# Kernel tuning notes

Measured on AMD Instinct MI355X. Metric: run time of the kernel, lower is better.

The kernel has to match this reference:

```python
import jax, jax.numpy as jnp
import numpy as np

T = 0.07  # temperature from __init__ default


def setup_inputs() -> dict:
    key = jax.random.key(0)
    ks = jax.random.split(key, 5)
    B, D, H, E = 4096, 2048, 2048, 128
    init = lambda k, shp, fan: jax.random.normal(k, shp, dtype=jnp.float32) * (1.0 / np.sqrt(fan))
    return {
        "input1": jax.random.normal(ks[0], (B, D), dtype=jnp.float32),
        "input2": jax.random.normal(ks[1], (B, D), dtype=jnp.float32),
        "W0": init(ks[2], (D, H), D), "b0": jnp.zeros((H,), jnp.float32),
        "W1": init(ks[3], (H, H), H), "b1": jnp.zeros((H,), jnp.float32),
        "W2": init(ks[4], (H, E), H), "b2": jnp.zeros((E,), jnp.float32),
    }


def _mlp(x, W0, b0, W1, b1, W2, b2):
    # Linear -> ReLU -> Linear -> Linear (ReLU only between hidden layers)
    x = jax.nn.relu(x @ W0 + b0)
    x = x @ W1 + b1
    return x @ W2 + b2


def reference(input1, input2, W0, b0, W1, b1, W2, b2):
    B = input1.shape[0]
    e1 = _mlp(input1, W0, b0, W1, b1, W2, b2)
    e2 = _mlp(input2, W0, b0, W1, b1, W2, b2)
    feats = jnp.stack([e1, e2], axis=1)                       # [B, 2, E]
    feats = feats / jnp.linalg.norm(feats, axis=2, keepdims=True)
    # view(N,2,dim).permute(1,0,2).reshape(2N,dim): view0 rows then view1 rows
    f = jnp.concatenate([feats[:, 0], feats[:, 1]], axis=0)   # [2B, E]
    N2 = 2 * B
    sim = (f @ f.T) / T                                        # [2B, 2B]
    idx = jnp.arange(N2)
    pos = sim[idx, (idx + B) % N2]                             # partner view similarity
    # exclude self-similarity (diagonal) from the logsumexp denominator
    sim = jnp.where(jnp.eye(N2, dtype=bool), jnp.float32(-1e9), sim)
    # CE with positive at index 0 of [pos, negatives] == -pos + logsumexp(non-self)
    loss = jnp.mean(jax.nn.logsumexp(sim, axis=1) - pos)
    return loss
```

## Files before the change

kernel.cpp:

```cpp
#include <hip/hip_runtime.h>
#include <stdint.h>

typedef float f32x4 __attribute__((ext_vector_type(4)));
typedef float f32x16 __attribute__((ext_vector_type(16)));
typedef __bf16 bf16x8 __attribute__((ext_vector_type(8)));
typedef unsigned short u16;
typedef unsigned int u32;

#define INVT 14.285714285714286f
#define L2E  1.4426950408889634f

__device__ __forceinline__ u16 f2bf(float f) {
  u32 u = __float_as_uint(f);
  u32 r = (u + 0x7fffu + ((u >> 16) & 1u)) >> 16;
  return (u16)r;
}
__device__ __forceinline__ float bf2f(u16 h) { return __uint_as_float(((u32)h) << 16); }

__device__ __forceinline__ void g2l16(const void* g, void* l) {
  auto gp = reinterpret_cast<__attribute__((address_space(1))) uint32_t*>(
      reinterpret_cast<uintptr_t>(g));
  auto lp = reinterpret_cast<__attribute__((address_space(3))) uint32_t*>(
      reinterpret_cast<uintptr_t>(l));
  __builtin_amdgcn_global_load_lds(gp, lp, 16, 0, 0);
}

__global__ __launch_bounds__(256) void k_prep(const float* __restrict__ in1,
                                              const float* __restrict__ in2,
                                              u16* __restrict__ Xb,
                                              const float* __restrict__ w0, u16* __restrict__ w0t,
                                              const float* __restrict__ w1, u16* __restrict__ w1t,
                                              const float* __restrict__ w2, u16* __restrict__ w2t) {
  const int bid = blockIdx.x;
  if (bid < 16384) {
    int i = (bid * 256 + threadIdx.x) * 4;
    float4 v;
    if (i < 8388608) v = *(const float4*)(in1 + i);
    else             v = *(const float4*)(in2 + (i - 8388608));
    ushort4 p;
    p.x = f2bf(v.x); p.y = f2bf(v.y); p.z = f2bf(v.z); p.w = f2bf(v.w);
    *(ushort4*)(Xb + i) = p;
    return;
  }
  __shared__ float t[64][65];
  const float* in; u16* out; int R, C, r0, c0;
  if (bid < 18432) {
    const int f = bid - 16384;
    const int z = f >> 10, rem = f & 1023;
    in = z ? w1 : w0; out = z ? w1t : w0t; R = 2048; C = 2048;
    r0 = (rem >> 5) * 64; c0 = (rem & 31) * 64;
  } else {
    const int f = bid - 18432;
    in = w2; out = w2t; R = 2048; C = 128;
    r0 = (f >> 1) * 64; c0 = (f & 1) * 64;
  }
#pragma unroll
  for (int p = 0; p < 16; ++p) {
    int idx = p * 256 + threadIdx.x;
    int r = idx >> 6, c = idx & 63;
    t[r][c] = in[(size_t)(r0 + r) * C + (c0 + c)];
  }
  __syncthreads();
#pragma unroll
  for (int p = 0; p < 16; ++p) {
    int idx = p * 256 + threadIdx.x;
    int c = idx >> 6, r = idx & 63;
    out[(size_t)(c0 + c) * R + (r0 + r)] = f2bf(t[r][c]);
  }
}

__global__ __launch_bounds__(256, 2) void k_gemm(const u16* __restrict__ A, const u16* __restrict__ Bt,
                                                 const float* __restrict__ bias, u16* __restrict__ C,
                                                 int M, int N, int K, int relu) {
  __shared__ __align__(16) u16 sm[36864];
  const int tid = threadIdx.x;
  const int l = tid & 63, w = tid >> 6;
  const int wm = w >> 1, wn = w & 1;
  const int m0 = blockIdx.y * 256, n0 = blockIdx.x * 128;

  const int kb = ((l & 3) ^ ((l >> 3) & 3)) * 16;
  const char* gA = (const char*)(A + (size_t)(m0 + w * 64 + (l >> 2)) * K) + kb;
  const char* gB = (const char*)(Bt + (size_t)(n0 + w * 32 + (l >> 2)) * K) + kb;
  const size_t chRows = (size_t)16 * K * 2;

  auto issue = [&](int kcB, int stg) {
    char* base = (char*)sm + stg * 24576;
    char* dA = base + (w * 4) * 1024 + l * 16;
    char* dB = base + 16384 + (w * 2) * 1024 + l * 16;
#pragma unroll
    for (int j = 0; j < 4; ++j) g2l16(gA + j * chRows + kcB, dA + j * 1024);
#pragma unroll
    for (int j = 0; j < 2; ++j) g2l16(gB + j * chRows + kcB, dB + j * 1024);
  };

  const int lm = l & 31;
  const int c0 = l >> 5;
  const int sw = (lm >> 1) & 3;

  f32x16 acc[4][2] = {};

  auto compute = [&](int stg) {
    const u16* As = sm + stg * 12288;
    const u16* Bs = As + 8192;
#pragma unroll
    for (int t = 0; t < 2; ++t) {
      const int cc = (((t << 1) + c0) ^ sw) * 8;
      bf16x8 a4[4], b2[2];
#pragma unroll
      for (int fm = 0; fm < 4; ++fm)
        a4[fm] = *(const bf16x8*)(As + (wm * 128 + fm * 32 + lm) * 32 + cc);
#pragma unroll
      for (int fn = 0; fn < 2; ++fn)
        b2[fn] = *(const bf16x8*)(Bs + (wn * 64 + fn * 32 + lm) * 32 + cc);
#pragma unroll
      for (int fm = 0; fm < 4; ++fm)
#pragma unroll
        for (int fn = 0; fn < 2; ++fn)
          acc[fm][fn] = __builtin_amdgcn_mfma_f32_32x32x16_bf16(a4[fm], b2[fn],
                                                                acc[fm][fn], 0, 0, 0);
    }
  };

  const int NK = K >> 5;
  issue(0, 0);
  issue(64, 1);
  int st = 0;
  for (int kt = 0; kt < NK; ++kt) {
    if (kt + 1 < NK) asm volatile("s_waitcnt vmcnt(6)" ::: "memory");
    else             asm volatile("s_waitcnt vmcnt(0)" ::: "memory");
    asm volatile("s_barrier" ::: "memory");
    if (kt + 2 < NK) {
      int stp = st + 2; if (stp >= 3) stp -= 3;
      issue((kt + 2) * 64, stp);
    }
    compute(st);
    ++st; if (st == 3) st = 0;
  }

  const int colb = n0 + wn * 64 + lm;
  const int rowb = m0 + wm * 128 + 4 * c0;
#pragma unroll
  for (int fn = 0; fn < 2; ++fn) {
    const float b = bias[colb + fn * 32];
#pragma unroll
    for (int fm = 0; fm < 4; ++fm)
#pragma unroll
      for (int g = 0; g < 4; ++g)
#pragma unroll
        for (int rr = 0; rr < 4; ++rr) {
          float v = acc[fm][fn][g * 4 + rr] + b;
          if (relu) v = fmaxf(v, 0.0f);
          C[(size_t)(rowb + fm * 32 + g * 8 + rr) * N + colb + fn * 32] = f2bf(v);
        }
  }
}

__global__ __launch_bounds__(256, 2) void k_gemm_sk(const u16* __restrict__ A, const u16* __restrict__ Bt,
                                                    float* __restrict__ Ep, int K, int Ksplit) {
  __shared__ __align__(16) u16 sm[24576];
  const int tid = threadIdx.x;
  const int l = tid & 63, w = tid >> 6;
  const int wm = w >> 1, wn = w & 1;
  const int m0 = blockIdx.y * 128;
  const int split = blockIdx.x;
  const int k0s = split * Ksplit;

  const int kb = ((l & 3) ^ ((l >> 3) & 3)) * 16;
  const char* gA = (const char*)(A + (size_t)(m0 + w * 16 + (l >> 2)) * K + k0s) + kb;
  const char* gB = (const char*)(Bt + (size_t)(w * 16 + (l >> 2)) * K + k0s) + kb;
  const size_t radv = (size_t)64 * K * 2;

  auto issue = [&](int kcB, int stg) {
    char* base = (char*)sm + stg * 16384;
    char* dA = base + w * 1024 + l * 16;
    char* dB = base + 8192 + w * 1024 + l * 16;
    g2l16(gA + kcB, dA);
    g2l16(gA + radv + kcB, dA + 4096);
    g2l16(gB + kcB, dB);
    g2l16(gB + radv + kcB, dB + 4096);
  };

  const int lm = l & 31;
  const int c0 = l >> 5;
  const int sw = (lm >> 1) & 3;

  f32x16 acc[2][2] = {};

  auto compute = [&](int stg) {
    const u16* As = sm + stg * 8192;
    const u16* Bs = As + 4096;
#pragma unroll
    for (int t = 0; t < 2; ++t) {
      const int cc = (((t << 1) + c0) ^ sw) * 8;
      bf16x8 a2[2], b2[2];
#pragma unroll
      for (int fm = 0; fm < 2; ++fm) a2[fm] = *(const bf16x8*)(As + (wm * 64 + fm * 32 + lm) * 32 + cc);
#pragma unroll
      for (int fn = 0; fn < 2; ++fn) b2[fn] = *(const bf16x8*)(Bs + (wn * 64 + fn * 32 + lm) * 32 + cc);
#pragma unroll
      for (int fm = 0; fm < 2; ++fm)
#pragma unroll
        for (int fn = 0; fn < 2; ++fn)
          acc[fm][fn] = __builtin_amdgcn_mfma_f32_32x32x16_bf16(a2[fm], b2[fn],
                                                                acc[fm][fn], 0, 0, 0);
    }
  };

  const int NK = Ksplit >> 5;
  issue(0, 0);
  issue(64, 1);
  int st = 0;
  for (int kt = 0; kt < NK; ++kt) {
    if (kt + 1 < NK) asm volatile("s_waitcnt vmcnt(4)" ::: "memory");
    else             asm volatile("s_waitcnt vmcnt(0)" ::: "memory");
    asm volatile("s_barrier" ::: "memory");
    if (kt + 2 < NK) {
      int stp = st + 2; if (stp >= 3) stp -= 3;
      issue((kt + 2) * 64, stp);
    }
    compute(st);
    ++st; if (st == 3) st = 0;
  }

  const int colb = wn * 64 + lm;
  const int rowb = m0 + wm * 64 + 4 * c0;
#pragma unroll
  for (int fn = 0; fn < 2; ++fn)
#pragma unroll
    for (int fm = 0; fm < 2; ++fm)
#pragma unroll
      for (int g = 0; g < 4; ++g)
#pragma unroll
        for (int rr = 0; rr < 4; ++rr)
          Ep[((size_t)split * 8192 + rowb + fm * 32 + g * 8 + rr) * 128 + colb + fn * 32] =
              acc[fm][fn][g * 4 + rr];
}

__global__ __launch_bounds__(256) void k_norm(const float* __restrict__ Ep,
                                              const float* __restrict__ b2, u16* __restrict__ F) {
  const int l = threadIdx.x & 63, w = threadIdx.x >> 6;
  const int row = blockIdx.x * 4 + w;
  const float2* base = (const float2*)Ep + (size_t)row * 64 + l;
  float x = 0.f, y = 0.f;
#pragma unroll
  for (int s = 0; s < 4; ++s) {
    float2 t = base[(size_t)s * (8192 * 64)];
    x += t.x; y += t.y;
  }
  x += b2[l * 2]; y += b2[l * 2 + 1];
  float sq = x * x + y * y;
#pragma unroll
  for (int off = 1; off < 64; off <<= 1) sq += __shfl_xor(sq, off);
  const float inv = 1.0f / sqrtf(sq);
  F[(size_t)row * 128 + l * 2] = f2bf(x * inv);
  F[(size_t)row * 128 + l * 2 + 1] = f2bf(y * inv);
}

__global__ __launch_bounds__(256, 2) void k_sim(const u16* __restrict__ F, float* __restrict__ Sp) {
  __shared__ __align__(16) u16 sm[32768];
  const int tid = threadIdx.x;
  const int l = tid & 63, w = tid >> 6;
  const int wm = w >> 1, wn = w & 1;
  const int lm = l & 31, c0 = l >> 5;
  const int r0 = blockIdx.y * 128;
  const int cb0 = blockIdx.x * 1024;

  u16* B0 = sm;
  u16* AB1 = sm + 16384;

  const int srow0 = tid >> 4;
  const int schunk = tid & 15;
  auto stage = [&](const u16* src, u16* dst) {
#pragma unroll
    for (int j = 0; j < 8; ++j) {
      const int row = j * 16 + srow0;
      const int lc = schunk ^ (row & 7);
      g2l16((const char*)(src + (size_t)row * 128) + lc * 16,
            (char*)dst + j * 4096 + tid * 16);
    }
  };

  stage(F + (size_t)r0 * 128, AB1);
  asm volatile("s_waitcnt vmcnt(0)" ::: "memory");
  __syncthreads();

  bf16x8 a[2][8];
#pragma unroll
  for (int fm = 0; fm < 2; ++fm) {
    const int ra = wm * 64 + fm * 32 + lm;
#pragma unroll
    for (int kf = 0; kf < 8; ++kf)
      a[fm][kf] = *(const bf16x8*)(AB1 + ra * 128 + (((kf << 1) + c0) ^ (ra & 7)) * 8);
  }
  asm volatile("s_waitcnt lgkmcnt(0)" ::: "memory");

  stage(F + (size_t)cb0 * 128, B0);

  const float S2 = INVT * L2E;
  const int rB = wn * 64 + lm;
  f32x16 runS[2] = {};

#pragma unroll 1
  for (int p = 0; p < 8; ++p) {
    asm volatile("s_waitcnt vmcnt(0)" ::: "memory");
    asm volatile("s_barrier" ::: "memory");
    if (p < 7) stage(F + (size_t)(cb0 + (p + 1) * 128) * 128, (p & 1) ? B0 : AB1);
    const u16* Bs = (p & 1) ? AB1 : B0;

    f32x16 acc[2][2] = {};
#pragma unroll
    for (int kf = 0; kf < 8; ++kf) {
      const int kc = (kf << 1) + c0;
      bf16x8 b0v = *(const bf16x8*)(Bs + rB * 128 + (kc ^ (rB & 7)) * 8);
      bf16x8 b1v = *(const bf16x8*)(Bs + (rB + 32) * 128 + (kc ^ ((rB + 32) & 7)) * 8);
      acc[0][0] = __builtin_amdgcn_mfma_f32_32x32x16_bf16(a[0][kf], b0v, acc[0][0], 0, 0, 0);
      acc[0][1] = __builtin_amdgcn_mfma_f32_32x32x16_bf16(a[0][kf], b1v, acc[0][1], 0, 0, 0);
      acc[1][0] = __builtin_amdgcn_mfma_f32_32x32x16_bf16(a[1][kf], b0v, acc[1][0], 0, 0, 0);
      acc[1][1] = __builtin_amdgcn_mfma_f32_32x32x16_bf16(a[1][kf], b1v, acc[1][1], 0, 0, 0);
    }

    const int cp = cb0 + p * 128;
    if (cp == r0) {
#pragma unroll
      for (int fm = 0; fm < 2; ++fm)
#pragma unroll
        for (int fn = 0; fn < 2; ++fn) {
          const int rcol = wn * 64 + fn * 32 + lm;
#pragma unroll
          for (int r = 0; r < 16; ++r) {
            const int rrow = wm * 64 + fm * 32 + (r & 3) + 8 * (r >> 2) + 4 * c0;
            float e = exp2f(fmaf(acc[fm][fn][r], S2, -S2));
            if (rrow == rcol) e = 0.f;
            runS[fm][r] += e;
          }
        }
    } else {
#pragma unroll
      for (int fm = 0; fm < 2; ++fm)
#pragma unroll
        for (int fn = 0; fn < 2; ++fn)
#pragma unroll
          for (int r = 0; r < 16; ++r)
            runS[fm][r] += exp2f(fmaf(acc[fm][fn][r], S2, -S2));
    }
  }

#pragma unroll
  for (int fm = 0; fm < 2; ++fm)
#pragma unroll
    for (int r = 0; r < 16; ++r) {
      float s = runS[fm][r];
      s += __shfl_xor(s, 1);
      s += __shfl_xor(s, 2);
      s += __shfl_xor(s, 4);
      s += __shfl_xor(s, 8);
      s += __shfl_xor(s, 16);
      runS[fm][r] = s;
    }

  __syncthreads();
  float* red = (float*)sm;
  if (wn == 0) {
    if (lm == 0) {
#pragma unroll
      for (int fm = 0; fm < 2; ++fm)
#pragma unroll
        for (int r = 0; r < 16; ++r)
          red[wm * 64 + fm * 32 + (r & 3) + 8 * (r >> 2) + 4 * c0] = runS[fm][r];
    }
  }
  __syncthreads();
  if (wn == 1 && lm == 0) {
#pragma unroll
    for (int fm = 0; fm < 2; ++fm)
#pragma unroll
      for (int r = 0; r < 16; ++r) {
        const int rr = wm * 64 + fm * 32 + (r & 3) + 8 * (r >> 2) + 4 * c0;
        Sp[(size_t)blockIdx.x * 8192 + r0 + rr] = red[rr] + runS[fm][r];
      }
  }
}

__global__ __launch_bounds__(256) void k_combine(const float* __restrict__ Sp,
                                                 const u16* __restrict__ F,
                                                 float* __restrict__ out) {
  const int r = blockIdx.x * 256 + threadIdx.x;
  float S = 0.f;
#pragma unroll
  for (int c = 0; c < 8; ++c) S += Sp[c * 8192 + r];
  const float lse = INVT + logf(S);
  const int par = (r + 4096) & 8191;
  const bf16x8* a = (const bf16x8*)(F + (size_t)r * 128);
  const bf16x8* b = (const bf16x8*)(F + (size_t)par * 128);
  float dot = 0.f;
#pragma unroll
  for (int k = 0; k < 16; ++k) {
    bf16x8 va = a[k], vb = b[k];
#pragma unroll
    for (int j = 0; j < 8; ++j) dot = fmaf((float)va[j], (float)vb[j], dot);
  }
  float contrib = lse - dot * INVT;
#pragma unroll
  for (int off = 1; off < 64; off <<= 1) contrib += __shfl_xor(contrib, off);
  if ((threadIdx.x & 63) == 0) atomicAdd(out, contrib * (1.0f / 8192.0f));
}

extern "C" void kernel_launch(void* const* d_in, const int* in_sizes, int n_in,
                              void* d_out, int out_size, void* d_ws, size_t ws_size,
                              hipStream_t stream) {
  const float* input1 = (const float*)d_in[0];
  const float* input2 = (const float*)d_in[1];
  const float* W0 = (const float*)d_in[2];
  const float* b0 = (const float*)d_in[3];
  const float* W1 = (const float*)d_in[4];
  const float* b1 = (const float*)d_in[5];
  const float* W2 = (const float*)d_in[6];
  const float* b2 = (const float*)d_in[7];
  float* out = (float*)d_out;
  char* ws = (char*)d_ws;

  u16* Xb = (u16*)(ws + 0);
  u16* H1 = (u16*)(ws + 33554432);
  u16* W0T = (u16*)(ws + 67108864);
  u16* W1T = (u16*)(ws + 75497472);
  float* Ep = (float*)(ws + 67108864);
  u16* W2T = (u16*)(ws + 83886080);
  float* Sp = (float*)(ws + 83886080);
  u16* Ff = (u16*)(ws + 84410368);
  u16* H2 = Xb;

  hipMemsetAsync(d_out, 0, sizeof(float), stream);
  k_prep<<<18496, 256, 0, stream>>>(input1, input2, Xb, W0, W0T, W1, W1T, W2, W2T);
  k_gemm<<<dim3(16, 32), 256, 0, stream>>>(Xb, W0T, b0, H1, 8192, 2048, 2048, 1);
  k_gemm<<<dim3(16, 32), 256, 0, stream>>>(H1, W1T, b1, H2, 8192, 2048, 2048, 0);
  k_gemm_sk<<<dim3(4, 64), 256, 0, stream>>>(H2, W2T, Ep, 2048, 512);
  k_norm<<<2048, 256, 0, stream>>>(Ep, b2, Ff);
  k_sim<<<dim3(8, 64), 256, 0, stream>>>(Ff, Sp);
  k_combine<<<32, 256, 0, stream>>>(Sp, Ff, out);
}
```

Baseline: 352.6 us.

## Enlarge GEMM tile to 256x256 with 8 waves and interleaved prefetch

The main bf16 GEMM moves from 256x128 tiles with 4 waves and a 3-stage K=32 pipeline to 256x256 tiles with 8 waves. It double-buffers K=64 slabs in 128KB of LDS and issues the next slab's loads in quarters between the MFMA groups. Wave priority is raised around the MFMAs so they are scheduled ahead of other work. The aim is more data reuse per tile and better overlap of loads with compute, at the cost of a 128KB LDS footprint, which likely limits residency to one block per CU, plus extra barriers per K step.

```diff
diff --git a/kernel.cpp b/kernel.cpp
--- a/kernel.cpp
+++ b/kernel.cpp
@@ -69,42 +69,48 @@
   }
 }
 
-__global__ __launch_bounds__(256, 2) void k_gemm(const u16* __restrict__ A, const u16* __restrict__ Bt,
+__global__ __launch_bounds__(512, 2) void k_gemm(const u16* __restrict__ A, const u16* __restrict__ Bt,
                                                  const float* __restrict__ bias, u16* __restrict__ C,
                                                  int M, int N, int K, int relu) {
-  __shared__ __align__(16) u16 sm[36864];
+  __shared__ __align__(16) u16 sm[65536];
   const int tid = threadIdx.x;
   const int l = tid & 63, w = tid >> 6;
-  const int wm = w >> 1, wn = w & 1;
-  const int m0 = blockIdx.y * 256, n0 = blockIdx.x * 128;
-
-  const int kb = ((l & 3) ^ ((l >> 3) & 3)) * 16;
-  const char* gA = (const char*)(A + (size_t)(m0 + w * 64 + (l >> 2)) * K) + kb;
-  const char* gB = (const char*)(Bt + (size_t)(n0 + w * 32 + (l >> 2)) * K) + kb;
-  const size_t chRows = (size_t)16 * K * 2;
-
-  auto issue = [&](int kcB, int stg) {
-    char* base = (char*)sm + stg * 24576;
-    char* dA = base + (w * 4) * 1024 + l * 16;
-    char* dB = base + 16384 + (w * 2) * 1024 + l * 16;
-#pragma unroll
-    for (int j = 0; j < 4; ++j) g2l16(gA + j * chRows + kcB, dA + j * 1024);
-#pragma unroll
-    for (int j = 0; j < 2; ++j) g2l16(gB + j * chRows + kcB, dB + j * 1024);
+  const int wm = w >> 2, wn = w & 3;
+  const int m0 = blockIdx.y * 256, n0 = blockIdx.x * 256;
+
+  const int srow = tid >> 2;
+  const int sq = (tid & 3) ^ ((tid >> 3) & 3);
+  const char* gA = (const char*)(A + (size_t)(m0 + srow) * K + sq * 8);
+  const char* gB = (const char*)(Bt + (size_t)(n0 + srow) * K + sq * 8);
+  const size_t rstep = (size_t)128 * K * 2;
+
+  auto issue_half = [&](int t, int part, int stg) {
+    const int h = part >> 1, isB = part & 1;
+    const char* g = (isB ? gB : gA) + (size_t)t * 128 + h * 64;
+    char* lb = (char*)sm + stg * 65536 + isB * 32768 + h * 16384 + w * 1024 + l * 16;
+    g2l16(g, lb);
+    g2l16(g + rstep, lb + 8192);
   };
 
-  const int lm = l & 31;
-  const int c0 = l >> 5;
+  const int lm = l & 31, c0 = l >> 5;
   const int sw = (lm >> 1) & 3;
-
   f32x16 acc[4][2] = {};
-
-  auto compute = [&](int stg) {
-    const u16* As = sm + stg * 12288;
-    const u16* Bs = As + 8192;
-#pragma unroll
-    for (int t = 0; t < 2; ++t) {
-      const int cc = (((t << 1) + c0) ^ sw) * 8;
+  const int NT = K >> 6;
+
+  issue_half(0, 0, 0); issue_half(0, 1, 0); issue_half(0, 2, 0); issue_half(0, 3, 0);
+  asm volatile("s_waitcnt vmcnt(4)" ::: "memory");
+  asm volatile("s_barrier" ::: "memory");
+
+  for (int kt = 0; kt < NT; ++kt) {
+    const u16* bcur = sm + (kt & 1) * 32768;
+    const int nstg = (kt & 1) ^ 1;
+    const bool pf = (kt + 1) < NT;
+
+#pragma unroll
+    for (int k = 0; k < 4; ++k) {
+      const u16* As = bcur + (k >> 1) * 8192;
+      const u16* Bs = bcur + 16384 + (k >> 1) * 8192;
+      const int cc = (((k & 1) * 2 + c0) ^ sw) * 8;
       bf16x8 a4[4], b2[2];
 #pragma unroll
       for (int fm = 0; fm < 4; ++fm)
@@ -112,29 +118,20 @@
 #pragma unroll
       for (int fn = 0; fn < 2; ++fn)
         b2[fn] = *(const bf16x8*)(Bs + (wn * 64 + fn * 32 + lm) * 32 + cc);
+      if (pf) issue_half(kt + 1, k, nstg);
+      asm volatile("s_barrier" ::: "memory");
+      asm volatile("s_waitcnt lgkmcnt(0)" ::: "memory");
+      __builtin_amdgcn_s_setprio(1);
 #pragma unroll
       for (int fm = 0; fm < 4; ++fm)
 #pragma unroll
         for (int fn = 0; fn < 2; ++fn)
           acc[fm][fn] = __builtin_amdgcn_mfma_f32_32x32x16_bf16(a4[fm], b2[fn],
                                                                 acc[fm][fn], 0, 0, 0);
-    }
-  };
-
-  const int NK = K >> 5;
-  issue(0, 0);
-  issue(64, 1);
-  int st = 0;
-  for (int kt = 0; kt < NK; ++kt) {
-    if (kt + 1 < NK) asm volatile("s_waitcnt vmcnt(6)" ::: "memory");
-    else             asm volatile("s_waitcnt vmcnt(0)" ::: "memory");
-    asm volatile("s_barrier" ::: "memory");
-    if (kt + 2 < NK) {
-      int stp = st + 2; if (stp >= 3) stp -= 3;
-      issue((kt + 2) * 64, stp);
-    }
-    compute(st);
-    ++st; if (st == 3) st = 0;
+      __builtin_amdgcn_s_setprio(0);
+      if (k & 1) asm volatile("s_waitcnt vmcnt(4)" ::: "memory");
+      asm volatile("s_barrier" ::: "memory");
+    }
   }
 
   const int colb = n0 + wn * 64 + lm;
@@ -431,8 +428,8 @@
 
   hipMemsetAsync(d_out, 0, sizeof(float), stream);
   k_prep<<<18496, 256, 0, stream>>>(input1, input2, Xb, W0, W0T, W1, W1T, W2, W2T);
-  k_gemm<<<dim3(16, 32), 256, 0, stream>>>(Xb, W0T, b0, H1, 8192, 2048, 2048, 1);
-  k_gemm<<<dim3(16, 32), 256, 0, stream>>>(H1, W1T, b1, H2, 8192, 2048, 2048, 0);
+  k_gemm<<<dim3(8, 32), 512, 0, stream>>>(Xb, W0T, b0, H1, 8192, 2048, 2048, 1);
+  k_gemm<<<dim3(8, 32), 512, 0, stream>>>(H1, W1T, b1, H2, 8192, 2048, 2048, 0);
   k_gemm_sk<<<dim3(4, 64), 256, 0, stream>>>(H2, W2T, Ep, 2048, 512);
   k_norm<<<2048, 256, 0, stream>>>(Ep, b2, Ff);
   k_sim<<<dim3(8, 64), 256, 0, stream>>>(Ff, Sp);
```

Measured after the change: 345.5 us. 2.0% less time.
